# Performance work log

Measured on AMD Instinct MI355X. Metric: run time of the kernel, lower is better.

The kernel has to match this reference:

```python
import jax, jax.numpy as jnp
import numpy as np

EPS = 1e-6
CHUNK = 128  # chunk size for the causal linear-attention scan


def elu_plus_one(x):
    return jax.nn.elu(x) + 1.0


def causal_linear_attention(q, k, v):
    # out_t = (sq_t @ cumsum_{j<=t} sk_j v_j^T) / (sq_t . cumsum_{j<=t} sk_j), clamped
    B, S, D = q.shape
    sq = elu_plus_one(q)
    sk = elu_plus_one(k)
    N = S // CHUNK
    # [N, B, C, D] chunked layout for scan over chunks
    sq_c = sq.reshape(B, N, CHUNK, D).transpose(1, 0, 2, 3)
    sk_c = sk.reshape(B, N, CHUNK, D).transpose(1, 0, 2, 3)
    v_c = v.reshape(B, N, CHUNK, D).transpose(1, 0, 2, 3)
    mask = jnp.tril(jnp.ones((CHUNK, CHUNK), dtype=q.dtype))  # inclusive causal

    def step(carry, inp):
        S_kv, z = carry  # [B,D,D], [B,D] running sums from previous chunks
        sqi, ski, vi = inp
        A = jnp.einsum('bid,bjd->bij', sqi, ski) * mask  # intra-chunk causal scores
        num = jnp.einsum('bij,bje->bie', A, vi) + jnp.einsum('bid,bde->bie', sqi, S_kv)
        den = A.sum(-1) + jnp.einsum('bid,bd->bi', sqi, z)
        out = num / jnp.clip(den, EPS, None)[..., None]
        S_kv = S_kv + jnp.einsum('bcd,bce->bde', ski, vi)
        z = z + ski.sum(axis=1)
        return (S_kv, z), out

    init = (jnp.zeros((B, D, D), q.dtype), jnp.zeros((B, D), q.dtype))
    _, outs = jax.lax.scan(step, init, (sq_c, sk_c, v_c))
    return outs.transpose(1, 0, 2, 3).reshape(B, S, D)


def setup_inputs() -> dict:
    key = jax.random.key(0)
    ks = jax.random.split(key, 8)
    B, S, D = 2, 2048, 1024
    scale = 1.0 / np.sqrt(D)  # realistic init scale for the D x D projections
    return {
        'hidden_states': jax.random.normal(ks[0], (B, S, D), jnp.float32),
        'w_q': jax.random.normal(ks[1], (D, D), jnp.float32) * scale,
        'w_k': jax.random.normal(ks[2], (D, D), jnp.float32) * scale,
        'w_v': jax.random.normal(ks[3], (D, D), jnp.float32) * scale,
        'w_o': jax.random.normal(ks[4], (D, D), jnp.float32) * scale,
        'gate': jnp.zeros((1,), jnp.float32),
        'memory': jax.random.uniform(ks[5], (D, D), jnp.float32) * 0.01,
        'memory_norm': jax.random.uniform(ks[6], (D,), jnp.float32),
    }


def reference(hidden_states, w_q, w_k, w_v, w_o, gate, memory, memory_norm):
    # Projections (torch Linear: x @ W^T)
    q = hidden_states @ w_q.T
    k = hidden_states @ w_k.T
    v = hidden_states @ w_v.T

    # Retrieve from compressive memory (single bank)
    sigma_q = elu_plus_one(q)
    a_mem = sigma_q @ memory
    norm = jnp.clip(sigma_q @ memory_norm, EPS, None)[..., None]
    active = (memory_norm.sum() >= EPS).astype(q.dtype)
    memory_output = active * (a_mem / norm)

    local_output = causal_linear_attention(q, k, v)

    g = jax.nn.sigmoid(gate)  # [1], broadcasts
    output = g * memory_output + (1.0 - g) * local_output
    return output @ w_o.T
```

## Files before the change

### kernel.cpp

```cpp
#include <hip/hip_runtime.h>
#include <cstddef>

#define EPSF 1e-6f

constexpr int D   = 1024;
constexpr int Bv  = 2;
constexpr int S   = 2048;
constexpr int M   = Bv * S;
constexpr int CH  = 256;
constexpr int NCH = S / CH;

constexpr int TSZ  = 128 * 64;
constexpr int TA64 = 64 * 64;

typedef __attribute__((ext_vector_type(8))) short short8;
typedef __attribute__((ext_vector_type(4))) float floatx4;

__device__ __forceinline__ float elu1(float x) { return x > 0.f ? x + 1.f : __expf(x); }
__device__ __forceinline__ float sigmoidf_(float x) { return 1.f / (1.f + __expf(-x)); }
__device__ __forceinline__ unsigned short f2bf(float x) {
    unsigned u = __float_as_uint(x);
    return (unsigned short)((u + 0x7fffu + ((u >> 16) & 1u)) >> 16);
}
__device__ __forceinline__ float bf2f(unsigned short h) {
    return __uint_as_float(((unsigned)h) << 16);
}
__device__ __forceinline__ float wave_reduce(float x) {
#pragma unroll
    for (int off = 32; off > 0; off >>= 1) x += __shfl_down(x, off);
    return x;
}

__device__ __forceinline__ void gl_lds16(const unsigned short* g, unsigned short* l) {
    __builtin_amdgcn_global_load_lds(
        (const __attribute__((address_space(1))) void*)g,
        (__attribute__((address_space(3))) void*)l, 16, 0, 0);
}


__device__ __forceinline__ void stage128x64(const unsigned short* g, int stride,
                                            unsigned short* lds, int wave, int lane) {
    const int base = (wave << 6) + lane;
    const int c8   = (lane & 7) ^ (lane >> 3);
#pragma unroll
    for (int q = 0; q < 4; ++q) {
        const int P   = (q << 8) + base;
        const int row = P >> 3;
        gl_lds16(g + (size_t)row * stride + (c8 << 3), lds + (q << 11) + (wave << 9));
    }
}

__device__ __forceinline__ void stage64x64(const unsigned short* g, int stride,
                                           unsigned short* lds, int wave, int lane) {
    const int base = (wave << 6) + lane;
    const int c8   = (lane & 7) ^ (lane >> 3);
#pragma unroll
    for (int q = 0; q < 2; ++q) {
        const int P   = (q << 8) + base;
        const int row = P >> 3;
        gl_lds16(g + (size_t)row * stride + (c8 << 3), lds + (q << 11) + (wave << 9));
    }
}

__device__ __forceinline__ void mfma_step(const unsigned short* As, const unsigned short* Bs,
                                          int wm, int wn, int fr, int g, floatx4 acc[4][4]) {
    const int x7 = fr & 7;
#pragma unroll
    for (int s = 0; s < 2; ++s) {
        const int off = ((g + 4 * s) ^ x7) << 3;
        short8 af[4], bf[4];
#pragma unroll
        for (int i = 0; i < 4; ++i) af[i] = *(const short8*)&As[(wm + i * 16 + fr) * 64 + off];
#pragma unroll
        for (int j = 0; j < 4; ++j) bf[j] = *(const short8*)&Bs[(wn + j * 16 + fr) * 64 + off];
#pragma unroll
        for (int i = 0; i < 4; ++i)
#pragma unroll
            for (int j = 0; j < 4; ++j)
                acc[i][j] = __builtin_amdgcn_mfma_f32_16x16x32_bf16(af[i], bf[j], acc[i][j], 0, 0, 0);
    }
}

__device__ __forceinline__ void mfma_step64d(const unsigned short* As, const unsigned short* Bs,
                                             int wm, int wn, int fr, int g,
                                             floatx4 acc[2][4], floatx4 accd[2], short8 bones) {
    const int x7 = fr & 7;
#pragma unroll
    for (int s = 0; s < 2; ++s) {
        const int off = ((g + 4 * s) ^ x7) << 3;
        short8 af[2], bf[4];
#pragma unroll
        for (int i = 0; i < 2; ++i) af[i] = *(const short8*)&As[(wm + i * 16 + fr) * 64 + off];
#pragma unroll
        for (int j = 0; j < 4; ++j) bf[j] = *(const short8*)&Bs[(wn + j * 16 + fr) * 64 + off];
#pragma unroll
        for (int i = 0; i < 2; ++i) {
#pragma unroll
            for (int j = 0; j < 4; ++j)
                acc[i][j] = __builtin_amdgcn_mfma_f32_16x16x32_bf16(af[i], bf[j], acc[i][j], 0, 0, 0);
            accd[i] = __builtin_amdgcn_mfma_f32_16x16x32_bf16(af[i], bones, accd[i], 0, 0, 0);
        }
    }
}

__device__ __forceinline__ void mfma_step64(const unsigned short* As, const unsigned short* Bs,
                                            int wm, int wn, int fr, int g, floatx4 acc[2][4]) {
    const int x7 = fr & 7;
#pragma unroll
    for (int s = 0; s < 2; ++s) {
        const int off = ((g + 4 * s) ^ x7) << 3;
        short8 af[2], bf[4];
#pragma unroll
        for (int i = 0; i < 2; ++i) af[i] = *(const short8*)&As[(wm + i * 16 + fr) * 64 + off];
#pragma unroll
        for (int j = 0; j < 4; ++j) bf[j] = *(const short8*)&Bs[(wn + j * 16 + fr) * 64 + off];
#pragma unroll
        for (int i = 0; i < 2; ++i)
#pragma unroll
            for (int j = 0; j < 4; ++j)
                acc[i][j] = __builtin_amdgcn_mfma_f32_16x16x32_bf16(af[i], bf[j], acc[i][j], 0, 0, 0);
    }
}

__device__ __forceinline__ void gemm_loop_db(const unsigned short* Ag, int strideA,
                                             const unsigned short* Bg, int strideB, int Kk,
                                             unsigned short* As, unsigned short* Bs,
                                             int wave, int lane, int wm, int wn, int fr, int g,
                                             floatx4 acc[4][4]) {
    __syncthreads();
    stage128x64(Ag, strideA, As, wave, lane);
    stage128x64(Bg, strideB, Bs, wave, lane);
    int buf = 0;
    for (int k0 = 64; k0 < Kk; k0 += 64) {
        __syncthreads();
        const int nb = buf ^ 1;
        stage128x64(Ag + k0, strideA, As + nb * TSZ, wave, lane);
        stage128x64(Bg + k0, strideB, Bs + nb * TSZ, wave, lane);
        mfma_step(As + buf * TSZ, Bs + buf * TSZ, wm, wn, fr, g, acc);
        buf = nb;
    }
    __syncthreads();
    mfma_step(As + buf * TSZ, Bs + buf * TSZ, wm, wn, fr, g, acc);
}

__device__ __forceinline__ void gemm_loop_db64d(const unsigned short* Ag, int strideA,
                                                const unsigned short* Bg, int strideB, int Kk,
                                                unsigned short* As, unsigned short* Bs,
                                                int wave, int lane, int wm, int wn, int fr, int g,
                                                floatx4 acc[2][4], floatx4 accd[2], short8 bones) {
    __syncthreads();
    stage64x64(Ag, strideA, As, wave, lane);
    stage128x64(Bg, strideB, Bs, wave, lane);
    int buf = 0;
    for (int k0 = 64; k0 < Kk; k0 += 64) {
        __syncthreads();
        const int nb = buf ^ 1;
        stage64x64(Ag + k0, strideA, As + nb * TA64, wave, lane);
        stage128x64(Bg + k0, strideB, Bs + nb * TSZ, wave, lane);
        mfma_step64d(As + buf * TA64, Bs + buf * TSZ, wm, wn, fr, g, acc, accd, bones);
        buf = nb;
    }
    __syncthreads();
    mfma_step64d(As + buf * TA64, Bs + buf * TSZ, wm, wn, fr, g, acc, accd, bones);
}

__device__ __forceinline__ void gemm_loop_db64(const unsigned short* Ag, int strideA,
                                               const unsigned short* Bg, int strideB, int Kk,
                                               unsigned short* As, unsigned short* Bs,
                                               int wave, int lane, int wm, int wn, int fr, int g,
                                               floatx4 acc[2][4]) {
    __syncthreads();
    stage64x64(Ag, strideA, As, wave, lane);
    stage128x64(Bg, strideB, Bs, wave, lane);
    int buf = 0;
    for (int k0 = 64; k0 < Kk; k0 += 64) {
        __syncthreads();
        const int nb = buf ^ 1;
        stage64x64(Ag + k0, strideA, As + nb * TA64, wave, lane);
        stage128x64(Bg + k0, strideB, Bs + nb * TSZ, wave, lane);
        mfma_step64(As + buf * TA64, Bs + buf * TSZ, wm, wn, fr, g, acc);
        buf = nb;
    }
    __syncthreads();
    mfma_step64(As + buf * TA64, Bs + buf * TSZ, wm, wn, fr, g, acc);
}

__global__ __launch_bounds__(256) void prep(const float* __restrict__ h,
                                            const float* __restrict__ w_q, const float* __restrict__ w_k,
                                            const float* __restrict__ w_v, const float* __restrict__ w_o,
                                            const float* __restrict__ memory,
                                            unsigned short* __restrict__ h_b,
                                            unsigned short* __restrict__ wq_b, unsigned short* __restrict__ wk_b,
                                            unsigned short* __restrict__ wv_b, unsigned short* __restrict__ wo_b,
                                            unsigned short* __restrict__ memT)
{
    __shared__ unsigned short T[64][72];
    const int id = blockIdx.x, tid = threadIdx.x;
    if (id < 4096) {
        const size_t i = ((size_t)id * 256 + tid) * 4;
        float4 v = *(const float4*)(h + i);
        ushort4 o; o.x = f2bf(v.x); o.y = f2bf(v.y); o.z = f2bf(v.z); o.w = f2bf(v.w);
        *(ushort4*)(h_b + i) = o;
    } else if (id < 8192) {
        const int t = id - 4096, which = t >> 10;
        const float* in = (which == 0) ? w_q : (which == 1) ? w_k : (which == 2) ? w_v : w_o;
        unsigned short* out = (which == 0) ? wq_b : (which == 1) ? wk_b : (which == 2) ? wv_b : wo_b;
        const size_t i = ((size_t)(t & 1023) * 256 + tid) * 4;
        float4 v = *(const float4*)(in + i);
        ushort4 o; o.x = f2bf(v.x); o.y = f2bf(v.y); o.z = f2bf(v.z); o.w = f2bf(v.w);
        *(ushort4*)(out + i) = o;
    } else {
        const int t = id - 8192;
        const int d0 = (t >> 4) * 64, e0 = (t & 15) * 64;
        const int r = tid >> 4, c4 = (tid & 15) * 4;
        for (int rr = r; rr < 64; rr += 16) {
            float4 v = *(const float4*)(memory + (size_t)(d0 + rr) * D + e0 + c4);
            T[rr][c4 + 0] = f2bf(v.x); T[rr][c4 + 1] = f2bf(v.y);
            T[rr][c4 + 2] = f2bf(v.z); T[rr][c4 + 3] = f2bf(v.w);
        }
        __syncthreads();
        for (int rr = r; rr < 64; rr += 16) {
            ushort4 o;
            o.x = T[c4 + 0][rr]; o.y = T[c4 + 1][rr];
            o.z = T[c4 + 2][rr]; o.w = T[c4 + 3][rr];
            *(ushort4*)(memT + (size_t)(e0 + rr) * D + d0 + c4) = o;
        }
    }
}

__global__ __launch_bounds__(256) void proj_fused(const unsigned short* __restrict__ h_b,
                                                  const unsigned short* __restrict__ wq,
                                                  const unsigned short* __restrict__ wk,
                                                  const unsigned short* __restrict__ wv,
                                                  unsigned short* __restrict__ sq,
                                                  unsigned short* __restrict__ sk,
                                                  unsigned short* __restrict__ v)
{
    __shared__ unsigned short As[2 * TSZ], Bs[2 * TSZ];
    const int id = blockIdx.x;
    const int x = id & 7, y = id >> 3;
    const int strip = x + 8 * (y % 12);
    const int n     = y / 12;
    const int sub = strip >> 5, m = strip & 31;
    const int m0 = m * 128, n0 = n * 128;
    const unsigned short* B = (sub == 0) ? wq : (sub == 1) ? wk : wv;
    unsigned short* C = (sub == 0) ? sq : (sub == 1) ? sk : v;

    const int tid = threadIdx.x, wave = tid >> 6, lane = tid & 63;
    const int wm = (wave >> 1) * 64, wn = (wave & 1) * 64;
    const int fr = lane & 15, g = lane >> 4;
    const int q4 = g * 4;

    floatx4 acc[4][4] = {};
    gemm_loop_db(h_b + (size_t)m0 * D, D, B + (size_t)n0 * D, D, D,
                 As, Bs, wave, lane, wm, wn, fr, g, acc);

#pragma unroll
    for (int i = 0; i < 4; ++i)
#pragma unroll
        for (int j = 0; j < 4; ++j) {
            const int col = n0 + wn + j * 16 + fr;
#pragma unroll
            for (int r = 0; r < 4; ++r) {
                const int row = m0 + wm + i * 16 + q4 + r;
                float val = acc[i][j][r];
                if (sub < 2) val = elu1(val);
                C[(size_t)row * D + col] = f2bf(val);
            }
        }
}

__global__ __launch_bounds__(256) void stage2(const unsigned short* __restrict__ sq,
                                              const unsigned short* __restrict__ sk,
                                              const unsigned short* __restrict__ memT,
                                              const unsigned short* __restrict__ v_b,
                                              const float* __restrict__ mnorm,
                                              const float* __restrict__ gate,
                                              unsigned short* __restrict__ combm,
                                              unsigned short* __restrict__ Sbuf2,
                                              unsigned short* __restrict__ vT,
                                              float* __restrict__ rowscale)
{
    __shared__ unsigned short As[2 * TSZ], Bs[2 * TSZ];
    const int id = blockIdx.x, tid = threadIdx.x;
    const int wave = tid >> 6, lane = tid & 63;
    const int wm = (wave >> 1) * 64, wn = (wave & 1) * 64;
    const int fr = lane & 15, g = lane >> 4;
    const int q4 = g * 4;

    if (id < 256) {
        const int x = id & 7, y = id >> 3;
        const int m0 = (x + 8 * (y & 3)) * 128;
        const int n0 = (y >> 2) * 128;
        floatx4 acc[4][4] = {};
        gemm_loop_db(sq + (size_t)m0 * D, D, memT + (size_t)n0 * D, D, D,
                     As, Bs, wave, lane, wm, wn, fr, g, acc);
#pragma unroll
        for (int i = 0; i < 4; ++i)
#pragma unroll
            for (int j = 0; j < 4; ++j) {
                const int col = n0 + wn + j * 16 + fr;
#pragma unroll
                for (int r = 0; r < 4; ++r)
                    combm[(size_t)(m0 + wm + i * 16 + q4 + r) * D + col] = f2bf(acc[i][j][r]);
            }
    } else if (id < 544) {
        const int t = id - 256;
        const int b = t / 144, rem = t % 144;
        const int p = rem >> 2, tt = rem & 3;
        const int it = tt >> 1, jt = tt & 1;
        int c = 0;
        while ((c + 1) * (c + 2) / 2 <= p) ++c;
        const int j = p - c * (c + 1) / 2;
        unsigned short* Srow0 = Sbuf2 + (size_t)(b * NCH + c) * CH * S;

        if (j == c && jt > it) {
            const int row = it * 128 + (tid >> 1);
            unsigned short* zp = Srow0 + (size_t)row * S + j * CH + jt * 128 + (tid & 1) * 64;
            uint4 z4 = make_uint4(0, 0, 0, 0);
#pragma unroll
            for (int i = 0; i < 8; ++i) *(uint4*)(zp + i * 8) = z4;
            return;
        }
        floatx4 acc[4][4] = {};
        gemm_loop_db(sq + ((size_t)b * S + (size_t)c * CH + it * 128) * D, D,
                     sk + ((size_t)b * S + (size_t)j * CH + jt * 128) * D, D, D,
                     As, Bs, wave, lane, wm, wn, fr, g, acc);
        const bool diag = (j == c && it == jt);
#pragma unroll
        for (int i = 0; i < 4; ++i)
#pragma unroll
            for (int jj = 0; jj < 4; ++jj) {
                const int col = jt * 128 + wn + jj * 16 + fr;
#pragma unroll
                for (int r = 0; r < 4; ++r) {
                    const int row = it * 128 + wm + i * 16 + q4 + r;
                    float val = acc[i][jj][r];
                    if (diag && col > row) val = 0.f;
                    Srow0[(size_t)row * S + j * CH + col] = f2bf(val);
                }
            }
    } else if (id < 1568) {
        unsigned short (*T)[72] = (unsigned short(*)[72])As;
        const int t = id - 544;
        const int b = t >> 9, rem = t & 511;
        const int s0 = (rem >> 4) * 64, d0 = (rem & 15) * 64;
        const int r = tid >> 4, c4 = (tid & 15) * 4;
        const unsigned short* ip = v_b + (size_t)b * S * D;
        for (int rr = r; rr < 64; rr += 16) {
            ushort4 vv = *(const ushort4*)(ip + (size_t)(s0 + rr) * D + d0 + c4);
            T[rr][c4 + 0] = vv.x; T[rr][c4 + 1] = vv.y; T[rr][c4 + 2] = vv.z; T[rr][c4 + 3] = vv.w;
        }
        __syncthreads();
        unsigned short* op = vT + (size_t)b * D * S;
        for (int rr = r; rr < 64; rr += 16) {
            ushort4 o;
            o.x = T[c4 + 0][rr]; o.y = T[c4 + 1][rr];
            o.z = T[c4 + 2][rr]; o.w = T[c4 + 3][rr];
            *(ushort4*)(op + (size_t)(d0 + rr) * S + s0 + c4) = o;
        }
    } else {
        const int row = (id - 1568) * 4 + wave;
        const unsigned short* sr = sq + (size_t)row * D;
        float dot = 0.f, msum = 0.f;
        for (int d = lane; d < D; d += 64) {
            float mn = mnorm[d];
            dot += bf2f(sr[d]) * mn;
            msum += mn;
        }
        dot = wave_reduce(dot);
        msum = wave_reduce(msum);
        if (lane == 0) {
            const float gg = sigmoidf_(gate[0]);
            const float active = (msum >= EPSF) ? 1.f : 0.f;
            rowscale[row] = gg * active / fmaxf(dot, EPSF);
        }
    }
}

__global__ __launch_bounds__(256) void pv64(const unsigned short* __restrict__ Sbuf2,
                                            const unsigned short* __restrict__ vT,
                                            const float* __restrict__ rowscale,
                                            const float* __restrict__ gate,
                                            unsigned short* __restrict__ combm)
{
    __shared__ unsigned short As2[2 * TA64], Bs2[2 * TSZ];
    const int id = blockIdx.x, tid = threadIdx.x;
    const int wave = tid >> 6, lane = tid & 63;
    const int wm = (wave >> 1) * 32, wn = (wave & 1) * 64;
    const int fr = lane & 15, g = lane >> 4;
    const int q4 = g * 4;

    const int x = id & 7, y = id >> 3;
    const int g_ = x + 8 * (y & 7);
    const int e  = y >> 3;
    const int b = g_ >> 5;
    const int rem = g_ & 31;
    const int c = (NCH - 1) - (rem >> 2);
    const int i0 = (rem & 3) * 64, e0 = e * 128;

    const short one_bf = (short)0x3F80;
    short8 bones = {one_bf, one_bf, one_bf, one_bf, one_bf, one_bf, one_bf, one_bf};

    floatx4 acc[2][4] = {};
    floatx4 accd[2] = {};
    gemm_loop_db64d(Sbuf2 + ((size_t)(b * NCH + c) * CH + i0) * S, S,
                    vT + (size_t)b * D * S + (size_t)e0 * S, S, (c + 1) * CH,
                    As2, Bs2, wave, lane, wm, wn, fr, g, acc, accd, bones);

    const float gg = sigmoidf_(gate[0]);
    const float wloc = 1.f - gg;
#pragma unroll
    for (int i = 0; i < 2; ++i)
#pragma unroll
        for (int j = 0; j < 4; ++j) {
            const int col = e0 + wn + j * 16 + fr;
#pragma unroll
            for (int r = 0; r < 4; ++r) {
                const int li = i0 + wm + i * 16 + q4 + r;
                const int rg = b * S + c * CH + li;
                const float inv = wloc / fmaxf(accd[i][r], EPSF);
                const size_t idx = (size_t)rg * D + col;
                combm[idx] = f2bf(bf2f(combm[idx]) * rowscale[rg] + acc[i][j][r] * inv);
            }
        }
}

__global__ __launch_bounds__(256) void outproj64(const unsigned short* __restrict__ A,
                                                 const unsigned short* __restrict__ wo,
                                                 float* __restrict__ out)
{
    __shared__ unsigned short As2[2 * TA64], Bs2[2 * TSZ];
    const int id = blockIdx.x, tid = threadIdx.x;
    const int wave = tid >> 6, lane = tid & 63;
    const int wm = (wave >> 1) * 32, wn = (wave & 1) * 64;
    const int fr = lane & 15, g = lane >> 4;
    const int q4 = g * 4;

    const int x = id & 7, y = id >> 3;
    const int m0 = (x + 8 * (y & 7)) * 64;
    const int n0 = (y >> 3) * 128;

    floatx4 acc[2][4] = {};
    gemm_loop_db64(A + (size_t)m0 * D, D, wo + (size_t)n0 * D, D, D,
                   As2, Bs2, wave, lane, wm, wn, fr, g, acc);

#pragma unroll
    for (int i = 0; i < 2; ++i)
#pragma unroll
        for (int j = 0; j < 4; ++j) {
            const int col = n0 + wn + j * 16 + fr;
#pragma unroll
            for (int r = 0; r < 4; ++r)
                out[(size_t)(m0 + wm + i * 16 + q4 + r) * D + col] = acc[i][j][r];
        }
}

extern "C" void kernel_launch(void* const* d_in, const int* in_sizes, int n_in,
                              void* d_out, int out_size, void* d_ws, size_t ws_size,
                              hipStream_t stream)
{
    const float* h      = (const float*)d_in[0];
    const float* w_q    = (const float*)d_in[1];
    const float* w_k    = (const float*)d_in[2];
    const float* w_v    = (const float*)d_in[3];
    const float* w_o    = (const float*)d_in[4];
    const float* gate   = (const float*)d_in[5];
    const float* memory = (const float*)d_in[6];
    const float* mnorm  = (const float*)d_in[7];
    float* out = (float*)d_out;

    unsigned short* h_b   = (unsigned short*)d_ws;
    unsigned short* wq_b  = h_b + (size_t)M * D;
    unsigned short* wk_b  = wq_b + (size_t)D * D;
    unsigned short* wv_b  = wk_b + (size_t)D * D;
    unsigned short* wo_b  = wv_b + (size_t)D * D;
    unsigned short* memT  = wo_b + (size_t)D * D;
    unsigned short* sq_b  = memT + (size_t)D * D;
    unsigned short* sk_b  = sq_b + (size_t)M * D;
    unsigned short* v_b   = sk_b + (size_t)M * D;
    unsigned short* vT    = v_b + (size_t)M * D;
    unsigned short* Sbuf2 = vT + (size_t)M * D;
    unsigned short* combm = Sbuf2 + (size_t)Bv * NCH * CH * S;
    float* rowscale = (float*)(combm + (size_t)M * D);

    dim3 blk(256);

    prep<<<8448, blk, 0, stream>>>(h, w_q, w_k, w_v, w_o, memory,
                                   h_b, wq_b, wk_b, wv_b, wo_b, memT);
    proj_fused<<<768, blk, 0, stream>>>(h_b, wq_b, wk_b, wv_b, sq_b, sk_b, v_b);
    stage2<<<2592, blk, 0, stream>>>(sq_b, sk_b, memT, v_b, mnorm, gate,
                                     combm, Sbuf2, vT, rowscale);
    pv64<<<512, blk, 0, stream>>>(Sbuf2, vT, rowscale, gate, combm);
    outproj64<<<512, blk, 0, stream>>>(combm, wo_b, out);
}
```

Measured before the change: 244.5 us.

## Triple-buffer K=32 GEMM pipeline, shrink pv/outproj tiles to 64x64, vectorize norm dot

The main 128x128 GEMMs move from a double-buffered K=64 loop to a triple-buffered K=32 loop. It uses explicit vmcnt waits, a raw barrier and setprio around the MFMA block so loads for two steps ahead overlap compute. The pv and out-projection kernels switch to 64x64 tiles with twice as many blocks to improve occupancy and tail balance. The memory-norm row dot product is vectorized with 16-byte loads. Risks are more barriers per K and lower per-block reuse from the smaller tiles.

New measurement: 204.3 us. -16.4%, faster.

```diff
diff --git a/kernel.cpp b/kernel.cpp
--- a/kernel.cpp
+++ b/kernel.cpp
@@ -10,8 +10,8 @@
 constexpr int CH  = 256;
 constexpr int NCH = S / CH;
 
-constexpr int TSZ  = 128 * 64;
-constexpr int TA64 = 64 * 64;
+constexpr int TSZ  = 128 * 32;
+constexpr int T66  = 64 * 64;
 
 typedef __attribute__((ext_vector_type(8))) short short8;
 typedef __attribute__((ext_vector_type(4))) float floatx4;
@@ -37,17 +37,14 @@
         (__attribute__((address_space(3))) void*)l, 16, 0, 0);
 }
 
-
-__device__ __forceinline__ void stage128x64(const unsigned short* g, int stride,
+__device__ __forceinline__ void stage128x32(const unsigned short* g, int stride,
                                             unsigned short* lds, int wave, int lane) {
-    const int base = (wave << 6) + lane;
-    const int c8   = (lane & 7) ^ (lane >> 3);
-#pragma unroll
-    for (int q = 0; q < 4; ++q) {
-        const int P   = (q << 8) + base;
-        const int row = P >> 3;
-        gl_lds16(g + (size_t)row * stride + (c8 << 3), lds + (q << 11) + (wave << 9));
-    }
+    const int t   = (wave << 6) + lane;
+    const int row = t >> 2;
+    const int cb  = (((t & 3) ^ ((row >> 1) & 3)) << 3);
+    unsigned short* l0 = lds + (wave << 9);
+    gl_lds16(g + (size_t)row * stride + cb, l0);
+    gl_lds16(g + (size_t)(row + 64) * stride + cb, l0 + 2048);
 }
 
 __device__ __forceinline__ void stage64x64(const unsigned short* g, int stride,
@@ -64,125 +61,128 @@
 
 __device__ __forceinline__ void mfma_step(const unsigned short* As, const unsigned short* Bs,
                                           int wm, int wn, int fr, int g, floatx4 acc[4][4]) {
-    const int x7 = fr & 7;
-#pragma unroll
-    for (int s = 0; s < 2; ++s) {
-        const int off = ((g + 4 * s) ^ x7) << 3;
-        short8 af[4], bf[4];
-#pragma unroll
-        for (int i = 0; i < 4; ++i) af[i] = *(const short8*)&As[(wm + i * 16 + fr) * 64 + off];
-#pragma unroll
-        for (int j = 0; j < 4; ++j) bf[j] = *(const short8*)&Bs[(wn + j * 16 + fr) * 64 + off];
-#pragma unroll
-        for (int i = 0; i < 4; ++i)
-#pragma unroll
-            for (int j = 0; j < 4; ++j)
-                acc[i][j] = __builtin_amdgcn_mfma_f32_16x16x32_bf16(af[i], bf[j], acc[i][j], 0, 0, 0);
-    }
-}
-
-__device__ __forceinline__ void mfma_step64d(const unsigned short* As, const unsigned short* Bs,
-                                             int wm, int wn, int fr, int g,
-                                             floatx4 acc[2][4], floatx4 accd[2], short8 bones) {
-    const int x7 = fr & 7;
-#pragma unroll
-    for (int s = 0; s < 2; ++s) {
-        const int off = ((g + 4 * s) ^ x7) << 3;
-        short8 af[2], bf[4];
-#pragma unroll
-        for (int i = 0; i < 2; ++i) af[i] = *(const short8*)&As[(wm + i * 16 + fr) * 64 + off];
-#pragma unroll
-        for (int j = 0; j < 4; ++j) bf[j] = *(const short8*)&Bs[(wn + j * 16 + fr) * 64 + off];
-#pragma unroll
-        for (int i = 0; i < 2; ++i) {
-#pragma unroll
-            for (int j = 0; j < 4; ++j)
-                acc[i][j] = __builtin_amdgcn_mfma_f32_16x16x32_bf16(af[i], bf[j], acc[i][j], 0, 0, 0);
-            accd[i] = __builtin_amdgcn_mfma_f32_16x16x32_bf16(af[i], bones, accd[i], 0, 0, 0);
-        }
-    }
-}
-
-__device__ __forceinline__ void mfma_step64(const unsigned short* As, const unsigned short* Bs,
-                                            int wm, int wn, int fr, int g, floatx4 acc[2][4]) {
-    const int x7 = fr & 7;
-#pragma unroll
-    for (int s = 0; s < 2; ++s) {
-        const int off = ((g + 4 * s) ^ x7) << 3;
-        short8 af[2], bf[4];
-#pragma unroll
-        for (int i = 0; i < 2; ++i) af[i] = *(const short8*)&As[(wm + i * 16 + fr) * 64 + off];
-#pragma unroll
-        for (int j = 0; j < 4; ++j) bf[j] = *(const short8*)&Bs[(wn + j * 16 + fr) * 64 + off];
-#pragma unroll
-        for (int i = 0; i < 2; ++i)
-#pragma unroll
-            for (int j = 0; j < 4; ++j)
-                acc[i][j] = __builtin_amdgcn_mfma_f32_16x16x32_bf16(af[i], bf[j], acc[i][j], 0, 0, 0);
-    }
-}
-
-__device__ __forceinline__ void gemm_loop_db(const unsigned short* Ag, int strideA,
-                                             const unsigned short* Bg, int strideB, int Kk,
+    const int off = ((g ^ ((fr >> 1) & 3)) << 3);
+    short8 af[4], bf[4];
+#pragma unroll
+    for (int i = 0; i < 4; ++i) af[i] = *(const short8*)&As[(wm + i * 16 + fr) * 32 + off];
+#pragma unroll
+    for (int j = 0; j < 4; ++j) bf[j] = *(const short8*)&Bs[(wn + j * 16 + fr) * 32 + off];
+#pragma unroll
+    for (int i = 0; i < 4; ++i)
+#pragma unroll
+        for (int j = 0; j < 4; ++j)
+            acc[i][j] = __builtin_amdgcn_mfma_f32_16x16x32_bf16(af[i], bf[j], acc[i][j], 0, 0, 0);
+}
+
+__device__ __forceinline__ void gemm_loop_tb(const unsigned short* __restrict__ Ag,
+                                             const unsigned short* __restrict__ Bg,
                                              unsigned short* As, unsigned short* Bs,
                                              int wave, int lane, int wm, int wn, int fr, int g,
                                              floatx4 acc[4][4]) {
+    const int NT = D / 32;
+    stage128x32(Ag, D, As, wave, lane);
+    stage128x32(Bg, D, Bs, wave, lane);
+    stage128x32(Ag + 32, D, As + TSZ, wave, lane);
+    stage128x32(Bg + 32, D, Bs + TSZ, wave, lane);
+    int cb = 0;
+    for (int u = 0; u < NT; ++u) {
+        if (u == NT - 1) asm volatile("s_waitcnt vmcnt(0)" ::: "memory");
+        else             asm volatile("s_waitcnt vmcnt(4)" ::: "memory");
+        __builtin_amdgcn_s_barrier();
+        asm volatile("" ::: "memory");
+        if (u + 2 < NT) {
+            int nb = cb + 2; if (nb >= 3) nb -= 3;
+            stage128x32(Ag + (u + 2) * 32, D, As + nb * TSZ, wave, lane);
+            stage128x32(Bg + (u + 2) * 32, D, Bs + nb * TSZ, wave, lane);
+        }
+        __builtin_amdgcn_s_setprio(1);
+        mfma_step(As + cb * TSZ, Bs + cb * TSZ, wm, wn, fr, g, acc);
+        __builtin_amdgcn_s_setprio(0);
+        if (++cb == 3) cb = 0;
+    }
+}
+
+__device__ __forceinline__ void mfma_6464d(const unsigned short* As, const unsigned short* Bs,
+                                           int wm, int wn, int fr, int g,
+                                           floatx4 acc[2][2], floatx4 accd[2], short8 bones) {
+    const int x7 = fr & 7;
+#pragma unroll
+    for (int s = 0; s < 2; ++s) {
+        const int off = ((g + 4 * s) ^ x7) << 3;
+        short8 af[2], bf[2];
+#pragma unroll
+        for (int i = 0; i < 2; ++i) af[i] = *(const short8*)&As[(wm + i * 16 + fr) * 64 + off];
+#pragma unroll
+        for (int j = 0; j < 2; ++j) bf[j] = *(const short8*)&Bs[(wn + j * 16 + fr) * 64 + off];
+#pragma unroll
+        for (int i = 0; i < 2; ++i) {
+#pragma unroll
+            for (int j = 0; j < 2; ++j)
+                acc[i][j] = __builtin_amdgcn_mfma_f32_16x16x32_bf16(af[i], bf[j], acc[i][j], 0, 0, 0);
+            accd[i] = __builtin_amdgcn_mfma_f32_16x16x32_bf16(af[i], bones, accd[i], 0, 0, 0);
+        }
+    }
+}
+
+__device__ __forceinline__ void mfma_6464(const unsigned short* As, const unsigned short* Bs,
+                                          int wm, int wn, int fr, int g, floatx4 acc[2][2]) {
+    const int x7 = fr & 7;
+#pragma unroll
+    for (int s = 0; s < 2; ++s) {
+        const int off = ((g + 4 * s) ^ x7) << 3;
+        short8 af[2], bf[2];
+#pragma unroll
+        for (int i = 0; i < 2; ++i) af[i] = *(const short8*)&As[(wm + i * 16 + fr) * 64 + off];
+#pragma unroll
+        for (int j = 0; j < 2; ++j) bf[j] = *(const short8*)&Bs[(wn + j * 16 + fr) * 64 + off];
+#pragma unroll
+        for (int i = 0; i < 2; ++i)
+#pragma unroll
+            for (int j = 0; j < 2; ++j)
+                acc[i][j] = __builtin_amdgcn_mfma_f32_16x16x32_bf16(af[i], bf[j], acc[i][j], 0, 0, 0);
+    }
+}
+
+__device__ __forceinline__ void gemm_loop_6464d(const unsigned short* Ag, int sA,
+                                                const unsigned short* Bg, int sB, int Kk,
+                                                unsigned short* As, unsigned short* Bs,
+                                                int wave, int lane, int wm, int wn, int fr, int g,
+                                                floatx4 acc[2][2], floatx4 accd[2], short8 bones) {
     __syncthreads();
-    stage128x64(Ag, strideA, As, wave, lane);
-    stage128x64(Bg, strideB, Bs, wave, lane);
+    stage64x64(Ag, sA, As, wave, lane);
+    stage64x64(Bg, sB, Bs, wave, lane);
     int buf = 0;
     for (int k0 = 64; k0 < Kk; k0 += 64) {
         __syncthreads();
         const int nb = buf ^ 1;
-        stage128x64(Ag + k0, strideA, As + nb * TSZ, wave, lane);
-        stage128x64(Bg + k0, strideB, Bs + nb * TSZ, wave, lane);
-        mfma_step(As + buf * TSZ, Bs + buf * TSZ, wm, wn, fr, g, acc);
+        stage64x64(Ag + k0, sA, As + nb * T66, wave, lane);
+        stage64x64(Bg + k0, sB, Bs + nb * T66, wave, lane);
+        mfma_6464d(As + buf * T66, Bs + buf * T66, wm, wn, fr, g, acc, accd, bones);
         buf = nb;
     }
     __syncthreads();
-    mfma_step(As + buf * TSZ, Bs + buf * TSZ, wm, wn, fr, g, acc);
-}
-
-__device__ __forceinline__ void gemm_loop_db64d(const unsigned short* Ag, int strideA,
-                                                const unsigned short* Bg, int strideB, int Kk,
-                                                unsigned short* As, unsigned short* Bs,
-                                                int wave, int lane, int wm, int wn, int fr, int g,
-                                                floatx4 acc[2][4], floatx4 accd[2], short8 bones) {
+    mfma_6464d(As + buf * T66, Bs + buf * T66, wm, wn, fr, g, acc, accd, bones);
+}
+
+__device__ __forceinline__ void gemm_loop_6464(const unsigned short* Ag, int sA,
+                                               const unsigned short* Bg, int sB, int Kk,
+                                               unsigned short* As, unsigned short* Bs,
+                                               int wave, int lane, int wm, int wn, int fr, int g,
+                                               floatx4 acc[2][2]) {
     __syncthreads();
-    stage64x64(Ag, strideA, As, wave, lane);
-    stage128x64(Bg, strideB, Bs, wave, lane);
+    stage64x64(Ag, sA, As, wave, lane);
+    stage64x64(Bg, sB, Bs, wave, lane);
     int buf = 0;
     for (int k0 = 64; k0 < Kk; k0 += 64) {
         __syncthreads();
         const int nb = buf ^ 1;
-        stage64x64(Ag + k0, strideA, As + nb * TA64, wave, lane);
-        stage128x64(Bg + k0, strideB, Bs + nb * TSZ, wave, lane);
-        mfma_step64d(As + buf * TA64, Bs + buf * TSZ, wm, wn, fr, g, acc, accd, bones);
+        stage64x64(Ag + k0, sA, As + nb * T66, wave, lane);
+        stage64x64(Bg + k0, sB, Bs + nb * T66, wave, lane);
+        mfma_6464(As + buf * T66, Bs + buf * T66, wm, wn, fr, g, acc);
         buf = nb;
     }
     __syncthreads();
-    mfma_step64d(As + buf * TA64, Bs + buf * TSZ, wm, wn, fr, g, acc, accd, bones);
-}
-
-__device__ __forceinline__ void gemm_loop_db64(const unsigned short* Ag, int strideA,
-                                               const unsigned short* Bg, int strideB, int Kk,
-                                               unsigned short* As, unsigned short* Bs,
-                                               int wave, int lane, int wm, int wn, int fr, int g,
-                                               floatx4 acc[2][4]) {
-    __syncthreads();
-    stage64x64(Ag, strideA, As, wave, lane);
-    stage128x64(Bg, strideB, Bs, wave, lane);
-    int buf = 0;
-    for (int k0 = 64; k0 < Kk; k0 += 64) {
-        __syncthreads();
-        const int nb = buf ^ 1;
-        stage64x64(Ag + k0, strideA, As + nb * TA64, wave, lane);
-        stage128x64(Bg + k0, strideB, Bs + nb * TSZ, wave, lane);
-        mfma_step64(As + buf * TA64, Bs + buf * TSZ, wm, wn, fr, g, acc);
-        buf = nb;
-    }
-    __syncthreads();
-    mfma_step64(As + buf * TA64, Bs + buf * TSZ, wm, wn, fr, g, acc);
+    mfma_6464(As + buf * T66, Bs + buf * T66, wm, wn, fr, g, acc);
 }
 
 __global__ __launch_bounds__(256) void prep(const float* __restrict__ h,
@@ -228,15 +228,15 @@
     }
 }
 
-__global__ __launch_bounds__(256) void proj_fused(const unsigned short* __restrict__ h_b,
-                                                  const unsigned short* __restrict__ wq,
-                                                  const unsigned short* __restrict__ wk,
-                                                  const unsigned short* __restrict__ wv,
-                                                  unsigned short* __restrict__ sq,
-                                                  unsigned short* __restrict__ sk,
-                                                  unsigned short* __restrict__ v)
+__global__ __launch_bounds__(256) void proj3(const unsigned short* __restrict__ h_b,
+                                             const unsigned short* __restrict__ wq,
+                                             const unsigned short* __restrict__ wk,
+                                             const unsigned short* __restrict__ wv,
+                                             unsigned short* __restrict__ sq,
+                                             unsigned short* __restrict__ sk,
+                                             unsigned short* __restrict__ v)
 {
-    __shared__ unsigned short As[2 * TSZ], Bs[2 * TSZ];
+    __shared__ unsigned short As[3 * TSZ], Bs[3 * TSZ];
     const int id = blockIdx.x;
     const int x = id & 7, y = id >> 3;
     const int strip = x + 8 * (y % 12);
@@ -252,7 +252,7 @@
     const int q4 = g * 4;
 
     floatx4 acc[4][4] = {};
-    gemm_loop_db(h_b + (size_t)m0 * D, D, B + (size_t)n0 * D, D, D,
+    gemm_loop_tb(h_b + (size_t)m0 * D, B + (size_t)n0 * D,
                  As, Bs, wave, lane, wm, wn, fr, g, acc);
 
 #pragma unroll
@@ -270,7 +270,7 @@
         }
 }
 
-__global__ __launch_bounds__(256) void stage2(const unsigned short* __restrict__ sq,
+__global__ __launch_bounds__(256) void stage3(const unsigned short* __restrict__ sq,
                                               const unsigned short* __restrict__ sk,
                                               const unsigned short* __restrict__ memT,
                                               const unsigned short* __restrict__ v_b,
@@ -281,7 +281,7 @@
                                               unsigned short* __restrict__ vT,
                                               float* __restrict__ rowscale)
 {
-    __shared__ unsigned short As[2 * TSZ], Bs[2 * TSZ];
+    __shared__ unsigned short As[3 * TSZ], Bs[3 * TSZ];
     const int id = blockIdx.x, tid = threadIdx.x;
     const int wave = tid >> 6, lane = tid & 63;
     const int wm = (wave >> 1) * 64, wn = (wave & 1) * 64;
@@ -293,7 +293,7 @@
         const int m0 = (x + 8 * (y & 3)) * 128;
         const int n0 = (y >> 2) * 128;
         floatx4 acc[4][4] = {};
-        gemm_loop_db(sq + (size_t)m0 * D, D, memT + (size_t)n0 * D, D, D,
+        gemm_loop_tb(sq + (size_t)m0 * D, memT + (size_t)n0 * D,
                      As, Bs, wave, lane, wm, wn, fr, g, acc);
 #pragma unroll
         for (int i = 0; i < 4; ++i)
@@ -323,8 +323,8 @@
             return;
         }
         floatx4 acc[4][4] = {};
-        gemm_loop_db(sq + ((size_t)b * S + (size_t)c * CH + it * 128) * D, D,
-                     sk + ((size_t)b * S + (size_t)j * CH + jt * 128) * D, D, D,
+        gemm_loop_tb(sq + ((size_t)b * S + (size_t)c * CH + it * 128) * D,
+                     sk + ((size_t)b * S + (size_t)j * CH + jt * 128) * D,
                      As, Bs, wave, lane, wm, wn, fr, g, acc);
         const bool diag = (j == c && it == jt);
 #pragma unroll
@@ -363,10 +363,17 @@
         const int row = (id - 1568) * 4 + wave;
         const unsigned short* sr = sq + (size_t)row * D;
         float dot = 0.f, msum = 0.f;
-        for (int d = lane; d < D; d += 64) {
-            float mn = mnorm[d];
-            dot += bf2f(sr[d]) * mn;
-            msum += mn;
+#pragma unroll
+        for (int p = 0; p < 2; ++p) {
+            const int d0 = p * 512 + lane * 8;
+            short8 sv = *(const short8*)(sr + d0);
+            float4 m0 = *(const float4*)(mnorm + d0);
+            float4 m1 = *(const float4*)(mnorm + d0 + 4);
+            dot += bf2f((unsigned short)sv[0]) * m0.x + bf2f((unsigned short)sv[1]) * m0.y
+                 + bf2f((unsigned short)sv[2]) * m0.z + bf2f((unsigned short)sv[3]) * m0.w
+                 + bf2f((unsigned short)sv[4]) * m1.x + bf2f((unsigned short)sv[5]) * m1.y
+                 + bf2f((unsigned short)sv[6]) * m1.z + bf2f((unsigned short)sv[7]) * m1.w;
+            msum += m0.x + m0.y + m0.z + m0.w + m1.x + m1.y + m1.z + m1.w;
         }
         dot = wave_reduce(dot);
         msum = wave_reduce(msum);
@@ -384,10 +391,10 @@
                                             const float* __restrict__ gate,
                                             unsigned short* __restrict__ combm)
 {
-    __shared__ unsigned short As2[2 * TA64], Bs2[2 * TSZ];
+    __shared__ unsigned short As2[2 * T66], Bs2[2 * T66];
     const int id = blockIdx.x, tid = threadIdx.x;
     const int wave = tid >> 6, lane = tid & 63;
-    const int wm = (wave >> 1) * 32, wn = (wave & 1) * 64;
+    const int wm = (wave >> 1) * 32, wn = (wave & 1) * 32;
     const int fr = lane & 15, g = lane >> 4;
     const int q4 = g * 4;
 
@@ -397,14 +404,14 @@
     const int b = g_ >> 5;
     const int rem = g_ & 31;
     const int c = (NCH - 1) - (rem >> 2);
-    const int i0 = (rem & 3) * 64, e0 = e * 128;
+    const int i0 = (rem & 3) * 64, e0 = e * 64;
 
     const short one_bf = (short)0x3F80;
     short8 bones = {one_bf, one_bf, one_bf, one_bf, one_bf, one_bf, one_bf, one_bf};
 
-    floatx4 acc[2][4] = {};
+    floatx4 acc[2][2] = {};
     floatx4 accd[2] = {};
-    gemm_loop_db64d(Sbuf2 + ((size_t)(b * NCH + c) * CH + i0) * S, S,
+    gemm_loop_6464d(Sbuf2 + ((size_t)(b * NCH + c) * CH + i0) * S, S,
                     vT + (size_t)b * D * S + (size_t)e0 * S, S, (c + 1) * CH,
                     As2, Bs2, wave, lane, wm, wn, fr, g, acc, accd, bones);
 
@@ -413,7 +420,7 @@
 #pragma unroll
     for (int i = 0; i < 2; ++i)
 #pragma unroll
-        for (int j = 0; j < 4; ++j) {
+        for (int j = 0; j < 2; ++j) {
             const int col = e0 + wn + j * 16 + fr;
 #pragma unroll
             for (int r = 0; r < 4; ++r) {
@@ -430,25 +437,25 @@
                                                  const unsigned short* __restrict__ wo,
                                                  float* __restrict__ out)
 {
-    __shared__ unsigned short As2[2 * TA64], Bs2[2 * TSZ];
+    __shared__ unsigned short As2[2 * T66], Bs2[2 * T66];
     const int id = blockIdx.x, tid = threadIdx.x;
     const int wave = tid >> 6, lane = tid & 63;
-    const int wm = (wave >> 1) * 32, wn = (wave & 1) * 64;
+    const int wm = (wave >> 1) * 32, wn = (wave & 1) * 32;
     const int fr = lane & 15, g = lane >> 4;
     const int q4 = g * 4;
 
     const int x = id & 7, y = id >> 3;
     const int m0 = (x + 8 * (y & 7)) * 64;
-    const int n0 = (y >> 3) * 128;
-
-    floatx4 acc[2][4] = {};
-    gemm_loop_db64(A + (size_t)m0 * D, D, wo + (size_t)n0 * D, D, D,
+    const int n0 = (y >> 3) * 64;
+
+    floatx4 acc[2][2] = {};
+    gemm_loop_6464(A + (size_t)m0 * D, D, wo + (size_t)n0 * D, D, D,
                    As2, Bs2, wave, lane, wm, wn, fr, g, acc);
 
 #pragma unroll
     for (int i = 0; i < 2; ++i)
 #pragma unroll
-        for (int j = 0; j < 4; ++j) {
+        for (int j = 0; j < 2; ++j) {
             const int col = n0 + wn + j * 16 + fr;
 #pragma unroll
             for (int r = 0; r < 4; ++r)
@@ -488,9 +495,9 @@
 
     prep<<<8448, blk, 0, stream>>>(h, w_q, w_k, w_v, w_o, memory,
                                    h_b, wq_b, wk_b, wv_b, wo_b, memT);
-    proj_fused<<<768, blk, 0, stream>>>(h_b, wq_b, wk_b, wv_b, sq_b, sk_b, v_b);
-    stage2<<<2592, blk, 0, stream>>>(sq_b, sk_b, memT, v_b, mnorm, gate,
+    proj3<<<768, blk, 0, stream>>>(h_b, wq_b, wk_b, wv_b, sq_b, sk_b, v_b);
+    stage3<<<2592, blk, 0, stream>>>(sq_b, sk_b, memT, v_b, mnorm, gate,
                                      combm, Sbuf2, vT, rowscale);
-    pv64<<<512, blk, 0, stream>>>(Sbuf2, vT, rowscale, gate, combm);
-    outproj64<<<512, blk, 0, stream>>>(combm, wo_b, out);
-}
+    pv64<<<1024, blk, 0, stream>>>(Sbuf2, vT, rowscale, gate, combm);
+    outproj64<<<1024, blk, 0, stream>>>(combm, wo_b, out);
+}
```
